# Kernel optimization log

Measured on AMD Instinct MI355X. Metric: run time of the kernel, lower is better.

Reference implementation:

```python
import jax, jax.numpy as jnp
import numpy as np
import math

B, N, D = 64, 512, 300
MASK_VALUE = -1.0e9
LN_EPS = 1e-5


def setup_inputs() -> dict:
    key = jax.random.key(0)
    ks = jax.random.split(key, 8)
    return {
        "concepts": jax.random.normal(ks[0], (B, N, D), dtype=jnp.float32),
        "ocr_tokens": jax.random.normal(ks[1], (B, N, D), dtype=jnp.float32),
        "ocr_mask": jax.random.randint(ks[2], (B, N, 1), 0, 2, dtype=jnp.int32),
        "wq": jax.random.normal(ks[3], (D, D), dtype=jnp.float32) * (1.0 / math.sqrt(D)),
        "bq": jax.random.normal(ks[4], (D,), dtype=jnp.float32) * 0.02,
        "wk": jax.random.normal(ks[5], (D, D), dtype=jnp.float32) * (1.0 / math.sqrt(D)),
        "bk": jax.random.normal(ks[6], (D,), dtype=jnp.float32) * 0.02,
        "ln_w": jnp.ones((D,), dtype=jnp.float32),
        "ln_b": jnp.zeros((D,), dtype=jnp.float32),
    }


def _layer_norm(x, w, b):
    mu = jnp.mean(x, axis=-1, keepdims=True)
    var = jnp.mean(jnp.square(x - mu), axis=-1, keepdims=True)
    return (x - mu) * jax.lax.rsqrt(var + LN_EPS) * w + b


def reference(concepts, ocr_tokens, ocr_mask, wq, bq, wk, bk, ln_w, ln_b):
    # Q/K linear projections (torch Linear: x @ W^T + b)
    Q = jnp.einsum('bnd,ed->bne', concepts, wq) + bq      # [B,N,D]
    K = jnp.einsum('bmd,ed->bme', ocr_tokens, wk) + bk    # [B,N,D]
    # scaled attention scores over concepts x ocr tokens
    A = jnp.einsum('bne,bme->bnm', Q, K) / math.sqrt(D)   # [B,N,N]
    P = jax.nn.softmax(A, axis=-1)
    semantic = jnp.einsum('bnm,bmd->bnd', P, concepts)    # [B,N,D]
    # post-attention masked_fill (faithful to original: fill AFTER attention)
    semantic = jnp.where(ocr_mask == 0, jnp.float32(MASK_VALUE), semantic)
    out = _layer_norm(ocr_tokens + semantic, ln_w, ln_b)  # [B,N,D]
    return out
```

## Files before the change

kernel.cpp:

```cpp
#include <hip/hip_runtime.h>
#include <math.h>

#define Bb 64
#define Nn 512
#define Dd 300

typedef __attribute__((ext_vector_type(8))) short bfrag;
typedef __attribute__((ext_vector_type(4))) float f4;
typedef __attribute__((ext_vector_type(4))) unsigned u4;
typedef __attribute__((ext_vector_type(2))) unsigned u2;

union BF { unsigned u[4]; bfrag v; u4 q; };

__device__ inline unsigned bfr(float x){
    union{float f;unsigned u;}v; v.f=x;
    return (v.u + 0x7FFFu + ((v.u>>16)&1u))>>16;
}
__device__ inline unsigned pk_rne(float a, float b){ return bfr(a) | (bfr(b)<<16); }
__device__ inline unsigned pk_tr(float a, float b){
    union{float f;unsigned u;} ua, ub; ua.f=a; ub.f=b;
    return (ua.u>>16) | (ub.u & 0xFFFF0000u);
}
__device__ inline char* wadr(char* dout, unsigned f){
    return dout + (size_t)(f>>9)*1200u + 608u + (f&511u);
}
__device__ inline void async16(const char* g, char* l){
    __builtin_amdgcn_global_load_lds(
        (const __attribute__((address_space(1))) void*)g,
        (__attribute__((address_space(3))) void*)l, 16, 0, 0);
}

#define TSZ 38400
#define VOFF 19200

__global__ __launch_bounds__(256)
void cast_cT(const float* __restrict__ concepts, char* __restrict__ tiles)
{
    const int t  = threadIdx.x;
    const int mt = blockIdx.x, b = blockIdx.y;
    char* vz = tiles + ((size_t)(b*16 + mt))*TSZ + VOFF;
    for (int task = t; task < 300; task += 256) {
        int m8 = task / 75, d4 = task - m8*75;
        const float* src = concepts + ((size_t)(b*Nn + mt*32 + m8*8))*Dd + d4*4;
        float4 r[8];
        #pragma unroll
        for (int i = 0; i < 8; ++i) r[i] = *(const float4*)(src + (size_t)i*Dd);
        #pragma unroll
        for (int dd = 0; dd < 4; ++dd) {
            int d = d4*4 + dd;
            float x[8];
            #pragma unroll
            for (int i = 0; i < 8; ++i)
                x[i] = (dd==0) ? r[i].x : (dd==1) ? r[i].y : (dd==2) ? r[i].z : r[i].w;
            u4 q; q.x = pk_rne(x[0],x[1]); q.y = pk_rne(x[2],x[3]);
                  q.z = pk_rne(x[4],x[5]); q.w = pk_rne(x[6],x[7]);
            char* dst = (d < 288)
                ? vz + (d>>4)*1024 + m8*256 + (d&15)*16
                : vz + 18432 + m8*192 + (d-288)*16;
            *(u4*)dst = q;
        }
    }
}

__global__ __launch_bounds__(256)
void wprep(const float* __restrict__ wq, const float* __restrict__ wk,
           char* __restrict__ dout)
{
    const int sel = blockIdx.x / 10, kc = blockIdx.x % 10;
    const float* W = sel ? wk : wq;
    const int n = blockIdx.y*152 + threadIdx.x;
    if (threadIdx.x < 152 && n < 304) {
        unsigned uu[16];
        #pragma unroll
        for (int j = 0; j < 16; ++j) uu[j] = 0;
        if (n < Dd) {
            const float* wr = W + (size_t)n*Dd + kc*32;
            int nv4 = (kc < 9) ? 8 : 3;
            #pragma unroll
            for (int i = 0; i < 8; ++i) {
                if (i < nv4) {
                    float4 v = *(const float4*)(wr + i*4);
                    uu[2*i  ] = pk_rne(v.x, v.y);
                    uu[2*i+1] = pk_rne(v.z, v.w);
                }
            }
        }
        unsigned fb = (unsigned)(sel*194560 + kc*19456 + n*16);
        #pragma unroll
        for (int g = 0; g < 4; ++g) {
            u4 q; q.x = uu[4*g+0]; q.y = uu[4*g+1]; q.z = uu[4*g+2]; q.w = uu[4*g+3];
            *(u4*)wadr(dout, fb + g*4864) = q;
        }
    }
}

__global__ __launch_bounds__(256)
void proj4(const float* __restrict__ concepts, const float* __restrict__ ocr,
           const float* __restrict__ bq, const float* __restrict__ bk,
           char* __restrict__ dout, char* __restrict__ tiles)
{
    __shared__ char Wl[2][19456];
    const int t = threadIdx.x;
    const int w = t >> 6, lane = t & 63, ln = lane & 15, quad = lane >> 4;
    const int sel = blockIdx.y;
    const float* X    = sel ? ocr : concepts;
    const float* bias = sel ? bk  : bq;
    const int r0w = blockIdx.x*64 + w*16;
    const float* xr = X + (size_t)(r0w + ln)*Dd;

    const unsigned selbase = (unsigned)sel*194560u;
    #define STAGE_W(buf, kc) \
        for (int c = w; c < 19; c += 4) \
            async16((const char*)wadr(dout, selbase + (unsigned)(kc)*19456u + c*1024u + lane*16u), \
                    &Wl[buf][c*1024 + lane*16]);

    f4 acc[19];
    #pragma unroll
    for (int i = 0; i < 19; ++i) acc[i] = (f4){0.f,0.f,0.f,0.f};

    STAGE_W(0, 0);
    __syncthreads();

    for (int kc = 0; kc < 10; ++kc) {
        const int cur = kc & 1;
        if (kc < 9) { STAGE_W(1 - cur, kc + 1); }
        BF a;
        if (kc < 9) {
            float4 v0 = *(const float4*)(xr + kc*32 + quad*8);
            float4 v1 = *(const float4*)(xr + kc*32 + quad*8 + 4);
            a.u[0]=pk_tr(v0.x,v0.y); a.u[1]=pk_tr(v0.z,v0.w);
            a.u[2]=pk_tr(v1.x,v1.y); a.u[3]=pk_tr(v1.z,v1.w);
        } else {
            a.u[0]=0; a.u[1]=0; a.u[2]=0; a.u[3]=0;
            if (quad == 0) {
                float4 v0 = *(const float4*)(xr + 288);
                float4 v1 = *(const float4*)(xr + 292);
                a.u[0]=pk_tr(v0.x,v0.y); a.u[1]=pk_tr(v0.z,v0.w);
                a.u[2]=pk_tr(v1.x,v1.y); a.u[3]=pk_tr(v1.z,v1.w);
            } else if (quad == 1) {
                float4 v0 = *(const float4*)(xr + 296);
                a.u[0]=pk_tr(v0.x,v0.y); a.u[1]=pk_tr(v0.z,v0.w);
            }
        }
        #pragma unroll
        for (int nt = 0; nt < 19; ++nt) {
            BF bfv; bfv.q = *(const u4*)&Wl[cur][quad*4864 + nt*256 + ln*16];
            acc[nt] = __builtin_amdgcn_mfma_f32_16x16x32_bf16(a.v, bfv.v, acc[nt], 0,0,0);
        }
        __syncthreads();
    }

    const float QSCALE = 0.057735026918962584f;
    #pragma unroll
    for (int nt = 0; nt < 19; ++nt) {
        int e = nt*16 + ln;
        if (sel == 0) {
            #pragma unroll
            for (int reg = 0; reg < 4; ++reg) {
                int r = r0w + quad*4 + reg;
                short val = (e < Dd) ? (short)bfr((acc[nt][reg] + bias[e])*QSCALE) : (short)0;
                *(short*)(dout + (size_t)r*1200 + e*2) = val;
            }
        } else if (e < Dd) {
            float bv = bias[e];
            #pragma unroll
            for (int reg = 0; reg < 4; ++reg) {
                int r = r0w + quad*4 + reg;
                int b = r >> 9, m = r & 511, mt = m >> 5, ml = m & 31;
                char* tile = tiles + ((size_t)(b*16 + mt))*TSZ;
                short val = (short)bfr(acc[nt][reg] + bv);
                if (e < 288)
                    *(short*)(tile + 768 + (e>>5)*2048 + ((e>>3)&3)*512 + ml*16 + (e&7)*2) = val;
                else
                    *(short*)(tile + ml*24 + (e-288)*2) = val;
            }
        }
    }
}

__global__ __launch_bounds__(256)
void attn5(char* __restrict__ dout, const char* __restrict__ tiles,
           const float* __restrict__ ocr, const int* __restrict__ mask,
           const float* __restrict__ lnw, const float* __restrict__ lnb)
{
    __shared__ char S[TSZ];
    const int t = threadIdx.x;
    const int w = t >> 6, lane = t & 63, ln = lane & 15, quad = lane >> 4;
    const int b = blockIdx.x, n0 = blockIdx.y*64;
    const int nlane = n0 + w*16 + ln;

    const char* qb = dout + (size_t)(b*Nn + nlane)*1200;
    bfrag qf[10];
    #pragma unroll
    for (int kc = 0; kc < 9; ++kc)
        qf[kc] = *(const bfrag*)(qb + kc*64 + quad*16);
    {
        BF z; z.u[0]=z.u[1]=z.u[2]=z.u[3]=0;
        if (quad < 2) z.q = *(const u4*)(qb + 576 + quad*16);
        qf[9] = z.v;
    }

    f4 oacc[19];
    #pragma unroll
    for (int i = 0; i < 19; ++i) oacc[i] = (f4){0.f,0.f,0.f,0.f};
    float lrun = 0.f;
    const char* tb = tiles + (size_t)b*16*TSZ;

    for (int mt = 0; mt < 16; ++mt) {
        if (mt > 0) __syncthreads();
        {
            const char* src = tb + (size_t)mt*TSZ;
            for (int c = w; c < 37; c += 4)
                async16(src + c*1024 + lane*16, &S[c*1024 + lane*16]);
            if (w == 1 && lane < 32)
                async16(src + 37*1024 + lane*16, &S[37*1024 + lane*16]);
        }
        __syncthreads();
        const char* Kz = S;
        const char* Vz = S + VOFF;

        f4 slo = (f4){0.f,0.f,0.f,0.f}, shi = (f4){0.f,0.f,0.f,0.f};
        #pragma unroll
        for (int kc = 0; kc < 9; ++kc) {
            bfrag alo = *(const bfrag*)(Kz + 768 + kc*2048 + quad*512 + ln*16);
            bfrag ahi = *(const bfrag*)(Kz + 768 + kc*2048 + quad*512 + 256 + ln*16);
            slo = __builtin_amdgcn_mfma_f32_16x16x32_bf16(alo, qf[kc], slo, 0,0,0);
            shi = __builtin_amdgcn_mfma_f32_16x16x32_bf16(ahi, qf[kc], shi, 0,0,0);
        }
        {
            BF alo, ahi;
            alo.u[0]=alo.u[1]=alo.u[2]=alo.u[3]=0;
            ahi.u[0]=ahi.u[1]=ahi.u[2]=ahi.u[3]=0;
            if (quad < 2) {
                u2 x0 = *(const u2*)(Kz + ln*24 + quad*16);
                u2 x1 = *(const u2*)(Kz + ln*24 + quad*16 + 8);
                alo.u[0]=x0.x; alo.u[1]=x0.y; alo.u[2]=x1.x; alo.u[3]=x1.y;
                u2 y0 = *(const u2*)(Kz + (16+ln)*24 + quad*16);
                u2 y1 = *(const u2*)(Kz + (16+ln)*24 + quad*16 + 8);
                ahi.u[0]=y0.x; ahi.u[1]=y0.y; ahi.u[2]=y1.x; ahi.u[3]=y1.y;
            }
            slo = __builtin_amdgcn_mfma_f32_16x16x32_bf16(alo.v, qf[9], slo, 0,0,0);
            shi = __builtin_amdgcn_mfma_f32_16x16x32_bf16(ahi.v, qf[9], shi, 0,0,0);
        }

        float elo[4], ehi[4], ls = 0.f;
        #pragma unroll
        for (int reg = 0; reg < 4; ++reg) {
            elo[reg] = __expf(slo[reg]);
            ehi[reg] = __expf(shi[reg]);
            ls += elo[reg] + ehi[reg];
        }
        ls += __shfl_xor(ls, 16);
        ls += __shfl_xor(ls, 32);
        lrun += ls;

        unsigned lo01 = pk_rne(elo[0], elo[1]), lo23 = pk_rne(elo[2], elo[3]);
        unsigned hi01 = pk_rne(ehi[0], ehi[1]), hi23 = pk_rne(ehi[2], ehi[3]);
        int sA = 2*(quad & 1)*16 + ln, sB = sA + 16;
        unsigned l0 = (unsigned)__shfl((int)lo01, sA);
        unsigned l1 = (unsigned)__shfl((int)lo23, sA);
        unsigned l2 = (unsigned)__shfl((int)lo01, sB);
        unsigned l3 = (unsigned)__shfl((int)lo23, sB);
        unsigned h0 = (unsigned)__shfl((int)hi01, sA);
        unsigned h1 = (unsigned)__shfl((int)hi23, sA);
        unsigned h2 = (unsigned)__shfl((int)hi01, sB);
        unsigned h3 = (unsigned)__shfl((int)hi23, sB);
        BF p;
        bool useHi = quad >= 2;
        p.u[0] = useHi ? h0 : l0; p.u[1] = useHi ? h1 : l1;
        p.u[2] = useHi ? h2 : l2; p.u[3] = useHi ? h3 : l3;

        #pragma unroll
        for (int nt = 0; nt < 18; ++nt) {
            bfrag vf = *(const bfrag*)(Vz + nt*1024 + lane*16);
            oacc[nt] = __builtin_amdgcn_mfma_f32_16x16x32_bf16(p.v, vf, oacc[nt], 0,0,0);
        }
        {
            BF vf; vf.u[0]=vf.u[1]=vf.u[2]=vf.u[3]=0;
            if (ln < 12) vf.q = *(const u4*)(Vz + 18432 + quad*192 + ln*16);
            oacc[18] = __builtin_amdgcn_mfma_f32_16x16x32_bf16(p.v, vf.v, oacc[18], 0,0,0);
        }
    }

    float invl[4];
    #pragma unroll
    for (int reg = 0; reg < 4; ++reg) invl[reg] = 1.0f / __shfl(lrun, quad*4 + reg);
    #pragma unroll
    for (int reg = 0; reg < 4; ++reg) {
        int r = b*Nn + n0 + w*16 + quad*4 + reg;
        int mr = mask[r];
        float xs[19], s = 0.f, ss = 0.f;
        #pragma unroll
        for (int nt = 0; nt < 19; ++nt) {
            int d = nt*16 + ln;
            float x = 0.f;
            if (d < Dd) x = oacc[nt][reg]*invl[reg] + ocr[(size_t)r*Dd + d];
            xs[nt] = x; s += x; ss += x*x;
        }
        #pragma unroll
        for (int off = 1; off < 16; off <<= 1) {
            s += __shfl_xor(s, off); ss += __shfl_xor(ss, off);
        }
        float mu   = s * (1.0f/Dd);
        float var  = ss * (1.0f/Dd) - mu*mu;
        float rstd = rsqrtf(var + 1e-5f);
        #pragma unroll
        for (int nt = 0; nt < 19; ++nt) {
            int d = nt*16 + ln;
            if (d < Dd) {
                float y = mr ? (xs[nt]-mu)*rstd*lnw[d] + lnb[d] : lnw[d] + lnb[d];
                *(float*)(dout + (size_t)r*1200 + d*4) = y;
            }
        }
    }
}

extern "C" void kernel_launch(void* const* d_in, const int* in_sizes, int n_in,
                              void* d_out, int out_size, void* d_ws, size_t ws_size,
                              hipStream_t stream)
{
    const float* concepts = (const float*)d_in[0];
    const float* ocr      = (const float*)d_in[1];
    const int*   mask     = (const int*)d_in[2];
    const float* wq  = (const float*)d_in[3];
    const float* bq  = (const float*)d_in[4];
    const float* wk  = (const float*)d_in[5];
    const float* bk  = (const float*)d_in[6];
    const float* lnw = (const float*)d_in[7];
    const float* lnb = (const float*)d_in[8];

    char* dout  = (char*)d_out;
    char* tiles = (char*)d_ws;

    cast_cT<<<dim3(16, 64), 256, 0, stream>>>(concepts, tiles);
    wprep  <<<dim3(20, 2),  256, 0, stream>>>(wq, wk, dout);
    proj4  <<<dim3(512, 2), 256, 0, stream>>>(concepts, ocr, bq, bk, dout, tiles);
    attn5  <<<dim3(64, 8),  256, 0, stream>>>(dout, tiles, ocr, mask, lnw, lnb);
}
```

Baseline: 231.8 us.

## Double-buffer K/V tiles in attention and merge prep kernels into one launch

The attention kernel now splits its shared-memory tile into two K buffers and a separate V buffer. The next K tile and the current V tile load asynchronously while the MFMAs run, instead of the whole tile loading before compute with a full barrier. It also raises wave priority around the MFMA sections and fuses the concept-cast and weight-prep kernels into one launch to save a kernel launch. Shared memory use grows slightly, and the extra barriers per step could limit how much overlap is gained.

```diff
diff --git a/kernel.cpp b/kernel.cpp
--- a/kernel.cpp
+++ b/kernel.cpp
@@ -32,64 +32,67 @@
 
 #define TSZ 38400
 #define VOFF 19200
+#define ZSZ 19200
 
 __global__ __launch_bounds__(256)
-void cast_cT(const float* __restrict__ concepts, char* __restrict__ tiles)
+void prep(const float* __restrict__ concepts, char* __restrict__ tiles,
+          const float* __restrict__ wq, const float* __restrict__ wk,
+          char* __restrict__ dout)
 {
+    const int bx = blockIdx.x;
     const int t  = threadIdx.x;
-    const int mt = blockIdx.x, b = blockIdx.y;
-    char* vz = tiles + ((size_t)(b*16 + mt))*TSZ + VOFF;
-    for (int task = t; task < 300; task += 256) {
-        int m8 = task / 75, d4 = task - m8*75;
-        const float* src = concepts + ((size_t)(b*Nn + mt*32 + m8*8))*Dd + d4*4;
-        float4 r[8];
-        #pragma unroll
-        for (int i = 0; i < 8; ++i) r[i] = *(const float4*)(src + (size_t)i*Dd);
-        #pragma unroll
-        for (int dd = 0; dd < 4; ++dd) {
-            int d = d4*4 + dd;
-            float x[8];
-            #pragma unroll
-            for (int i = 0; i < 8; ++i)
-                x[i] = (dd==0) ? r[i].x : (dd==1) ? r[i].y : (dd==2) ? r[i].z : r[i].w;
-            u4 q; q.x = pk_rne(x[0],x[1]); q.y = pk_rne(x[2],x[3]);
-                  q.z = pk_rne(x[4],x[5]); q.w = pk_rne(x[6],x[7]);
-            char* dst = (d < 288)
-                ? vz + (d>>4)*1024 + m8*256 + (d&15)*16
-                : vz + 18432 + m8*192 + (d-288)*16;
-            *(u4*)dst = q;
-        }
-    }
-}
-
-__global__ __launch_bounds__(256)
-void wprep(const float* __restrict__ wq, const float* __restrict__ wk,
-           char* __restrict__ dout)
-{
-    const int sel = blockIdx.x / 10, kc = blockIdx.x % 10;
-    const float* W = sel ? wk : wq;
-    const int n = blockIdx.y*152 + threadIdx.x;
-    if (threadIdx.x < 152 && n < 304) {
-        unsigned uu[16];
-        #pragma unroll
-        for (int j = 0; j < 16; ++j) uu[j] = 0;
-        if (n < Dd) {
-            const float* wr = W + (size_t)n*Dd + kc*32;
-            int nv4 = (kc < 9) ? 8 : 3;
-            #pragma unroll
-            for (int i = 0; i < 8; ++i) {
-                if (i < nv4) {
-                    float4 v = *(const float4*)(wr + i*4);
-                    uu[2*i  ] = pk_rne(v.x, v.y);
-                    uu[2*i+1] = pk_rne(v.z, v.w);
+    if (bx < 1024) {
+        const int mt = bx & 15, b = bx >> 4;
+        char* vz = tiles + ((size_t)(b*16 + mt))*TSZ + VOFF;
+        for (int task = t; task < 300; task += 256) {
+            int m8 = task / 75, d4 = task - m8*75;
+            const float* src = concepts + ((size_t)(b*Nn + mt*32 + m8*8))*Dd + d4*4;
+            float4 r[8];
+            #pragma unroll
+            for (int i = 0; i < 8; ++i) r[i] = *(const float4*)(src + (size_t)i*Dd);
+            #pragma unroll
+            for (int dd = 0; dd < 4; ++dd) {
+                int d = d4*4 + dd;
+                float x[8];
+                #pragma unroll
+                for (int i = 0; i < 8; ++i)
+                    x[i] = (dd==0) ? r[i].x : (dd==1) ? r[i].y : (dd==2) ? r[i].z : r[i].w;
+                u4 q; q.x = pk_rne(x[0],x[1]); q.y = pk_rne(x[2],x[3]);
+                      q.z = pk_rne(x[4],x[5]); q.w = pk_rne(x[6],x[7]);
+                char* dst = (d < 288)
+                    ? vz + (d>>4)*1024 + m8*256 + (d&15)*16
+                    : vz + 18432 + m8*192 + (d-288)*16;
+                *(u4*)dst = q;
+            }
+        }
+    } else {
+        const int wid = bx - 1024;
+        const int xx = wid % 20, yy = wid / 20;
+        const int sel = xx / 10, kc = xx % 10;
+        const float* W = sel ? wk : wq;
+        const int n = yy*152 + t;
+        if (t < 152 && n < 304) {
+            unsigned uu[16];
+            #pragma unroll
+            for (int j = 0; j < 16; ++j) uu[j] = 0;
+            if (n < Dd) {
+                const float* wr = W + (size_t)n*Dd + kc*32;
+                int nv4 = (kc < 9) ? 8 : 3;
+                #pragma unroll
+                for (int i = 0; i < 8; ++i) {
+                    if (i < nv4) {
+                        float4 v = *(const float4*)(wr + i*4);
+                        uu[2*i  ] = pk_rne(v.x, v.y);
+                        uu[2*i+1] = pk_rne(v.z, v.w);
+                    }
                 }
             }
-        }
-        unsigned fb = (unsigned)(sel*194560 + kc*19456 + n*16);
-        #pragma unroll
-        for (int g = 0; g < 4; ++g) {
-            u4 q; q.x = uu[4*g+0]; q.y = uu[4*g+1]; q.z = uu[4*g+2]; q.w = uu[4*g+3];
-            *(u4*)wadr(dout, fb + g*4864) = q;
+            unsigned fb = (unsigned)(sel*194560 + kc*19456 + n*16);
+            #pragma unroll
+            for (int g = 0; g < 4; ++g) {
+                u4 q; q.x = uu[4*g+0]; q.y = uu[4*g+1]; q.z = uu[4*g+2]; q.w = uu[4*g+3];
+                *(u4*)wadr(dout, fb + g*4864) = q;
+            }
         }
     }
 }
@@ -179,11 +182,13 @@
 }
 
 __global__ __launch_bounds__(256)
-void attn5(char* __restrict__ dout, const char* __restrict__ tiles,
+void attn6(char* __restrict__ dout, const char* __restrict__ tiles,
            const float* __restrict__ ocr, const int* __restrict__ mask,
            const float* __restrict__ lnw, const float* __restrict__ lnb)
 {
-    __shared__ char S[TSZ];
+    __shared__ __align__(16) char Kb0[ZSZ];
+    __shared__ __align__(16) char Kb1[ZSZ];
+    __shared__ __align__(16) char Vb[ZSZ];
     const int t = threadIdx.x;
     const int w = t >> 6, lane = t & 63, ln = lane & 15, quad = lane >> 4;
     const int b = blockIdx.x, n0 = blockIdx.y*64;
@@ -206,20 +211,21 @@
     float lrun = 0.f;
     const char* tb = tiles + (size_t)b*16*TSZ;
 
-    for (int mt = 0; mt < 16; ++mt) {
-        if (mt > 0) __syncthreads();
-        {
-            const char* src = tb + (size_t)mt*TSZ;
-            for (int c = w; c < 37; c += 4)
-                async16(src + c*1024 + lane*16, &S[c*1024 + lane*16]);
-            if (w == 1 && lane < 32)
-                async16(src + 37*1024 + lane*16, &S[37*1024 + lane*16]);
-        }
-        __syncthreads();
-        const char* Kz = S;
-        const char* Vz = S + VOFF;
+#define STAGE_ZONE(SRC, DST) do { \
+        const char* s_ = (SRC); char* d_ = (DST); \
+        for (int c = w; c < 19; c += 4) \
+            if (c < 18 || lane < 48) \
+                async16(s_ + c*1024 + lane*16, d_ + c*1024 + lane*16); \
+    } while (0)
+
+    STAGE_ZONE(tb, Kb0);
+    __syncthreads();
+
+    auto step = [&](int mt, const char* Kz, char* Kw) {
+        STAGE_ZONE(tb + (size_t)mt*TSZ + VOFF, Vb);
 
         f4 slo = (f4){0.f,0.f,0.f,0.f}, shi = (f4){0.f,0.f,0.f,0.f};
+        __builtin_amdgcn_s_setprio(1);
         #pragma unroll
         for (int kc = 0; kc < 9; ++kc) {
             bfrag alo = *(const bfrag*)(Kz + 768 + kc*2048 + quad*512 + ln*16);
@@ -242,6 +248,7 @@
             slo = __builtin_amdgcn_mfma_f32_16x16x32_bf16(alo.v, qf[9], slo, 0,0,0);
             shi = __builtin_amdgcn_mfma_f32_16x16x32_bf16(ahi.v, qf[9], shi, 0,0,0);
         }
+        __builtin_amdgcn_s_setprio(0);
 
         float elo[4], ehi[4], ls = 0.f;
         #pragma unroll
@@ -270,16 +277,29 @@
         p.u[0] = useHi ? h0 : l0; p.u[1] = useHi ? h1 : l1;
         p.u[2] = useHi ? h2 : l2; p.u[3] = useHi ? h3 : l3;
 
+        __syncthreads();
+
+        if (mt < 15) STAGE_ZONE(tb + (size_t)(mt+1)*TSZ, Kw);
+
+        __builtin_amdgcn_s_setprio(1);
         #pragma unroll
         for (int nt = 0; nt < 18; ++nt) {
-            bfrag vf = *(const bfrag*)(Vz + nt*1024 + lane*16);
+            bfrag vf = *(const bfrag*)(Vb + nt*1024 + lane*16);
             oacc[nt] = __builtin_amdgcn_mfma_f32_16x16x32_bf16(p.v, vf, oacc[nt], 0,0,0);
         }
         {
             BF vf; vf.u[0]=vf.u[1]=vf.u[2]=vf.u[3]=0;
-            if (ln < 12) vf.q = *(const u4*)(Vz + 18432 + quad*192 + ln*16);
+            if (ln < 12) vf.q = *(const u4*)(Vb + 18432 + quad*192 + ln*16);
             oacc[18] = __builtin_amdgcn_mfma_f32_16x16x32_bf16(p.v, vf.v, oacc[18], 0,0,0);
         }
+        __builtin_amdgcn_s_setprio(0);
+
+        __syncthreads();
+    };
+
+    for (int mt2 = 0; mt2 < 16; mt2 += 2) {
+        step(mt2,     Kb0, Kb1);
+        step(mt2 + 1, Kb1, Kb0);
     }
 
     float invl[4];
@@ -332,8 +352,7 @@
     char* dout  = (char*)d_out;
     char* tiles = (char*)d_ws;
 
-    cast_cT<<<dim3(16, 64), 256, 0, stream>>>(concepts, tiles);
-    wprep  <<<dim3(20, 2),  256, 0, stream>>>(wq, wk, dout);
-    proj4  <<<dim3(512, 2), 256, 0, stream>>>(concepts, ocr, bq, bk, dout, tiles);
-    attn5  <<<dim3(64, 8),  256, 0, stream>>>(dout, tiles, ocr, mask, lnw, lnb);
-}
+    prep <<<dim3(1064),    256, 0, stream>>>(concepts, tiles, wq, wk, dout);
+    proj4<<<dim3(512, 2),  256, 0, stream>>>(concepts, ocr, bq, bk, dout, tiles);
+    attn6<<<dim3(64, 8),   256, 0, stream>>>(dout, tiles, ocr, mask, lnw, lnb);
+}
```

Result: no change. 231.9 us (+0.0%).
